# Optimization experiments

Measured on AMD Instinct MI355X. Metric: run time of the kernel, lower is better.

The kernel has to match this reference:

```python
import jax, jax.numpy as jnp
import numpy as np

GRID = 4096
WINDOW_SIZES = (128, 256, 512)  # self.window_schedule in the torch module
BLOCK_FRAC = 0.2                # fraction of blocked (fixed) cells


def setup_inputs() -> dict:
    key = jax.random.key(0)
    u = jax.random.uniform(key, (GRID, GRID), dtype=jnp.float32)
    # blocked cells > 0.0, free cells == 0.0 (binary fixed-cell occupancy mask)
    mask = (u > (1.0 - BLOCK_FRAC)).astype(jnp.float32)
    # the torch code requires the grid center (or an 8-neighbor) to be free;
    # force it free so the seed location is static.
    mask = mask.at[GRID // 2, GRID // 2].set(0.0)
    return {"fixed_cell_mask": mask}


def _dilate4(r):
    # 4-connected dilation of a boolean map (matches BFS neighbor set)
    up = jnp.pad(r[1:, :], ((0, 1), (0, 0)))
    dn = jnp.pad(r[:-1, :], ((1, 0), (0, 0)))
    lf = jnp.pad(r[:, 1:], ((0, 0), (0, 1)))
    rt = jnp.pad(r[:, :-1], ((0, 0), (1, 0)))
    return r | up | dn | lf | rt


def _flood_fill(free, cx, cy):
    """Parallel label-propagation equivalent of the serial BFS flood fill:
    reachable set of `free` cells 4-connected to seed (cx, cy). The seed is
    always tagged, exactly as in get_contiguous_free_region_in_window."""
    seed = jnp.zeros(free.shape, dtype=bool).at[cx, cy].set(True)

    def cond(state):
        reach, prev_count = state
        return jnp.sum(reach) != prev_count

    def body(state):
        reach, _ = state
        new = (_dilate4(reach) & free) | seed
        return new, jnp.sum(reach)

    reach, _ = jax.lax.while_loop(cond, body, (seed, jnp.int32(-1)))
    return reach


def reference(fixed_cell_mask):
    """Faithful JAX version of assemble_free_region_masks: for each window
    size, extract the centered window, flood-fill the contiguous free region
    from the center, and scatter it back into a full-grid boolean mask.
    Returns (masks [len(WINDOW_SIZES), H, W] float32, counts [len] int32)."""
    H, W = fixed_cell_mask.shape
    cx, cy = H // 2, W // 2  # seed is free by construction (see setup_inputs)
    masks, counts = [], []
    for size in WINDOW_SIZES:
        half = size // 2
        sx, ex = max(0, cx - half), min(H, cx + half)
        sy, ey = max(0, cy - half), min(W, cy + half)
        window = fixed_cell_mask[sx:ex, sy:ey]
        free = window == 0.0
        reach = _flood_fill(free, cx - sx, cy - sy)
        full = jnp.zeros((H, W), dtype=bool).at[sx:ex, sy:ey].set(reach)
        masks.append(full)
        counts.append(jnp.sum(reach))
    return jnp.stack(masks).astype(jnp.float32), jnp.stack(counts).astype(jnp.int32)
```

## Files before the change

kernel.cpp:

```cpp
#include <hip/hip_runtime.h>
#include <stdint.h>

#define GRID_N 4096
#define CELL_BLOCKS 1344
#define TILE_BLOCKS 336
#define NUM_EDGES 19712
#define EDGE_BLOCKS 77
#define ZERO_BLOCKS 8192

typedef float vfloat4 __attribute__((ext_vector_type(4)));

__device__ inline void decode_block(int b, int& w, int& S, int& lg, int& off,
                                    int& woff, int& baseblk) {
    if (b < 64)       { w = 0; S = 128; lg = 7; off = 1984; woff = 0;     baseblk = 0;   }
    else if (b < 320) { w = 1; S = 256; lg = 8; off = 1920; woff = 16384; baseblk = 64;  }
    else              { w = 2; S = 512; lg = 9; off = 1792; woff = 81920; baseblk = 320; }
}

__device__ inline void decode_tile(int b, int& S, int& lg, int& off, int& woff,
                                   int& tileR, int& tileC) {
    int t, tsh;
    if (b < 16)      { S = 128; lg = 7; off = 1984; woff = 0;     t = b;      tsh = 2; }
    else if (b < 80) { S = 256; lg = 8; off = 1920; woff = 16384; t = b - 16; tsh = 3; }
    else             { S = 512; lg = 9; off = 1792; woff = 81920; t = b - 80; tsh = 4; }
    tileR = t >> tsh;
    tileC = t & ((1 << tsh) - 1);
}

__device__ inline int uf_find(int* L, int a) {
    while (true) {
        int p = __hip_atomic_load(&L[a], __ATOMIC_RELAXED, __HIP_MEMORY_SCOPE_AGENT);
        if (p == a) return a;
        int gp = __hip_atomic_load(&L[p], __ATOMIC_RELAXED, __HIP_MEMORY_SCOPE_AGENT);
        if (gp == p) return p;
        __hip_atomic_compare_exchange_strong(&L[a], &p, gp,
            __ATOMIC_RELAXED, __ATOMIC_RELAXED, __HIP_MEMORY_SCOPE_AGENT);
        a = gp;
    }
}
__device__ inline void uf_union(int* L, int a, int b) {
    while (true) {
        a = uf_find(L, a);
        b = uf_find(L, b);
        if (a == b) return;
        if (a < b) { int t = a; a = b; b = t; }
        int old = atomicMin(&L[a], b);
        if (old == a) return;
        a = old;
    }
}

__device__ inline int lfind(int* lab, int a) {
    int p = __hip_atomic_load(&lab[a], __ATOMIC_RELAXED, __HIP_MEMORY_SCOPE_WORKGROUP);
    while (p != a) {
        a = p;
        p = __hip_atomic_load(&lab[a], __ATOMIC_RELAXED, __HIP_MEMORY_SCOPE_WORKGROUP);
    }
    return a;
}
__device__ inline void lunion(int* lab, int a, int b) {
    while (true) {
        a = lfind(lab, a);
        b = lfind(lab, b);
        if (a == b) return;
        if (a < b) { int t = a; a = b; b = t; }
        int old = atomicMin(&lab[a], b);
        if (old == a) return;
        a = old;
    }
}

__global__ void k_local(const float* __restrict__ mask, int* __restrict__ L) {
    int S, lg, off, woff, tileR, tileC;
    decode_tile(blockIdx.x, S, lg, off, woff, tileR, tileC);
    __shared__ int lab[1024];

    #pragma unroll
    for (int k = 0; k < 4; k++) {
        int l = threadIdx.x + k * 256;
        int lr = l >> 5, lc = l & 31;
        size_t g = (size_t)(off + tileR * 32 + lr) * GRID_N
                 + (size_t)(off + tileC * 32 + lc);
        lab[l] = (mask[g] == 0.0f) ? l : -1;
    }
    __syncthreads();

    #pragma unroll
    for (int k = 0; k < 4; k++) {
        int l = threadIdx.x + k * 256;
        if (lab[l] == -1) continue;
        int lr = l >> 5, lc = l & 31;
        if (lc + 1 < 32 && lab[l + 1] != -1)  lunion(lab, l, l + 1);
        if (lr + 1 < 32 && lab[l + 32] != -1) lunion(lab, l, l + 32);
    }
    __syncthreads();

    #pragma unroll
    for (int k = 0; k < 4; k++) {
        int l = threadIdx.x + k * 256;
        int lr = l >> 5, lc = l & 31;
        int gidx = (tileR * 32 + lr) * S + tileC * 32 + lc;
        if (lab[l] == -1) {
            L[woff + gidx] = -1;
        } else {
            int r = lfind(lab, l);
            int rr = r >> 5, rc = r & 31;
            L[woff + gidx] = (tileR * 32 + rr) * S + tileC * 32 + rc;
        }
    }
}

__global__ void k_zero_merge(int* __restrict__ L, float* __restrict__ out,
                             int out_size) {
    int b = blockIdx.x;
    if (b < EDGE_BLOCKS) {
        int e = b * 256 + threadIdx.x;
        int S, lg, woff, i; bool vert;
        if (e < 768)        { S = 128; lg = 7; woff = 0;     vert = e < 384;   i = vert ? e : e - 384; }
        else if (e < 4352)  { S = 256; lg = 8; woff = 16384; vert = e < 2560;  i = vert ? e - 768 : e - 2560; }
        else                { S = 512; lg = 9; woff = 81920; vert = e < 12032; i = vert ? e - 4352 : e - 12032; }
        int line = i >> lg;
        int pos = i & (S - 1);
        int* Lw = L + woff;
        int a, n;
        if (vert) { int c = line * 32 + 31; a = pos * S + c; n = a + 1; }
        else      { int r = line * 32 + 31; a = r * S + pos; n = a + S; }
        int la = Lw[a];
        int ln = Lw[n];
        int pla = __shfl_up(la, 1);
        int pln = __shfl_up(ln, 1);
        bool first = ((pos & 31) == 0);
        if (la != -1 && ln != -1 && (first || la != pla || ln != pln))
            uf_union(Lw, la, ln);
    } else {
        long long n4 = (long long)(out_size >> 2);
        long long i = (long long)(b - EDGE_BLOCKS) * 256 + threadIdx.x;
        long long stride = (long long)ZERO_BLOCKS * 256;
        vfloat4* o4 = (vfloat4*)out;
        vfloat4 z = (vfloat4)(0.0f);
        for (; i < n4; i += stride) __builtin_nontemporal_store(z, &o4[i]);
        long long t = (long long)(b - EDGE_BLOCKS) * 256 + threadIdx.x;
        long long tail = (long long)out_size - n4 * 4;
        if (t < tail) out[n4 * 4 + t] = 0.0f;
    }
}

__global__ void k_write(int* __restrict__ L, float* __restrict__ out) {
    int b = blockIdx.x;
    int w, S, lg, off, woff, baseblk;
    decode_block(b, w, S, lg, off, woff, baseblk);
    int idx = (b - baseblk) * 256 + threadIdx.x;
    int* Lw = L + woff;

    __shared__ int rootC;
    __shared__ float wsum[4];
    if (threadIdx.x == 0) {
        int centerIdx = (S >> 1) * S + (S >> 1);
        rootC = uf_find(Lw, centerIdx);
    }
    __syncthreads();

    int lab = Lw[idx];
    bool reach = false;
    if (lab != -1) {
        int root = uf_find(Lw, idx);
        reach = (root == rootC);
    }
    int r = idx >> lg;
    int c = idx & (S - 1);
    size_t go = (size_t)w * GRID_N * GRID_N + (size_t)(off + r) * GRID_N + (size_t)(off + c);
    out[go] = reach ? 1.0f : 0.0f;

    unsigned long long m = __ballot(reach);
    int lane = threadIdx.x & 63;
    int wv = threadIdx.x >> 6;
    if (lane == 0) wsum[wv] = (float)__popcll(m);
    __syncthreads();
    if (threadIdx.x == 0) {
        float s = wsum[0] + wsum[1] + wsum[2] + wsum[3];
        atomicAdd(&out[(size_t)3 * GRID_N * GRID_N + w], s);
    }
}

extern "C" void kernel_launch(void* const* d_in, const int* in_sizes, int n_in,
                              void* d_out, int out_size, void* d_ws, size_t ws_size,
                              hipStream_t stream) {
    const float* mask = (const float*)d_in[0];
    float* out = (float*)d_out;
    int* L = (int*)d_ws;

    k_local<<<TILE_BLOCKS, 256, 0, stream>>>(mask, L);
    k_zero_merge<<<EDGE_BLOCKS + ZERO_BLOCKS, 256, 0, stream>>>(L, out, out_size);
    k_write<<<CELL_BLOCKS, 256, 0, stream>>>(L, out);
}
```

Baseline: 274.3 us.

## Fuse CCL, merge, zero-fill and write into one cooperative kernel

Replaces the three separate launches with one cooperative kernel of 1024 blocks, using grid-wide syncs between the local labeling plus zero-fill phase, the edge merge phase and the write phase. It also adds path compression to the shared-memory find. The aim is to remove launch gaps and inter-kernel idle time. The trade-offs are fewer blocks doing the large zero-fill, the overhead of the grid barriers, and the cooperative launch's limit on residency.

```diff
diff --git a/kernel.cpp b/kernel.cpp
--- a/kernel.cpp
+++ b/kernel.cpp
@@ -1,14 +1,19 @@
 #include <hip/hip_runtime.h>
+#include <hip/hip_cooperative_groups.h>
 #include <stdint.h>
 
 #define GRID_N 4096
+#define NBLK 1024
+#define CCL_BLOCKS 336
 #define CELL_BLOCKS 1344
+#define NUM_EDGES 19712
 #define TILE_BLOCKS 336
-#define NUM_EDGES 19712
 #define EDGE_BLOCKS 77
 #define ZERO_BLOCKS 8192
 
 typedef float vfloat4 __attribute__((ext_vector_type(4)));
+
+namespace cg = cooperative_groups;
 
 __device__ inline void decode_block(int b, int& w, int& S, int& lg, int& off,
                                     int& woff, int& baseblk) {
@@ -51,12 +56,15 @@
 }
 
 __device__ inline int lfind(int* lab, int a) {
-    int p = __hip_atomic_load(&lab[a], __ATOMIC_RELAXED, __HIP_MEMORY_SCOPE_WORKGROUP);
-    while (p != a) {
-        a = p;
-        p = __hip_atomic_load(&lab[a], __ATOMIC_RELAXED, __HIP_MEMORY_SCOPE_WORKGROUP);
-    }
-    return a;
+    while (true) {
+        int p = __hip_atomic_load(&lab[a], __ATOMIC_RELAXED, __HIP_MEMORY_SCOPE_WORKGROUP);
+        if (p == a) return a;
+        int gp = __hip_atomic_load(&lab[p], __ATOMIC_RELAXED, __HIP_MEMORY_SCOPE_WORKGROUP);
+        if (gp == p) return p;
+        __hip_atomic_compare_exchange_strong(&lab[a], &p, gp,
+            __ATOMIC_RELAXED, __ATOMIC_RELAXED, __HIP_MEMORY_SCOPE_WORKGROUP);
+        a = gp;
+    }
 }
 __device__ inline void lunion(int* lab, int a, int b) {
     while (true) {
@@ -70,11 +78,124 @@
     }
 }
 
+__global__ __launch_bounds__(256, 4)
+void k_fused(const float* __restrict__ mask, int* __restrict__ L,
+             float* __restrict__ out, int out_size) {
+    __shared__ int lab[1024];
+    __shared__ int rootC;
+    __shared__ float wsum[4];
+    const int b = blockIdx.x;
+    const int tid = threadIdx.x;
+
+    if (b < CCL_BLOCKS) {
+        int S, lg, off, woff, tileR, tileC;
+        decode_tile(b, S, lg, off, woff, tileR, tileC);
+        (void)lg;
+        #pragma unroll
+        for (int k = 0; k < 4; k++) {
+            int l = tid + k * 256;
+            int lr = l >> 5, lc = l & 31;
+            size_t g = (size_t)(off + tileR * 32 + lr) * GRID_N
+                     + (size_t)(off + tileC * 32 + lc);
+            lab[l] = (mask[g] == 0.0f) ? l : -1;
+        }
+        __syncthreads();
+        #pragma unroll
+        for (int k = 0; k < 4; k++) {
+            int l = tid + k * 256;
+            if (lab[l] == -1) continue;
+            int lr = l >> 5, lc = l & 31;
+            if (lc + 1 < 32 && lab[l + 1] != -1)  lunion(lab, l, l + 1);
+            if (lr + 1 < 32 && lab[l + 32] != -1) lunion(lab, l, l + 32);
+        }
+        __syncthreads();
+        #pragma unroll
+        for (int k = 0; k < 4; k++) {
+            int l = tid + k * 256;
+            int lr = l >> 5, lc = l & 31;
+            int gidx = (tileR * 32 + lr) * S + tileC * 32 + lc;
+            if (lab[l] == -1) {
+                L[woff + gidx] = -1;
+            } else {
+                int r = lfind(lab, l);
+                int rr = r >> 5, rc = r & 31;
+                L[woff + gidx] = (tileR * 32 + rr) * S + tileC * 32 + rc;
+            }
+        }
+    } else {
+        long long n4 = (long long)(out_size >> 2);
+        long long i = (long long)(b - CCL_BLOCKS) * 256 + tid;
+        const long long stride = (long long)(NBLK - CCL_BLOCKS) * 256;
+        vfloat4* o4 = (vfloat4*)out;
+        vfloat4 z = (vfloat4)(0.0f);
+        for (; i < n4; i += stride) __builtin_nontemporal_store(z, &o4[i]);
+        long long t = (long long)(b - CCL_BLOCKS) * 256 + tid;
+        long long tail = (long long)out_size - n4 * 4;
+        if (t < tail) out[n4 * 4 + t] = 0.0f;
+    }
+    __threadfence();
+    cg::this_grid().sync();
+
+    {
+        int e = b * 256 + tid;
+        if (e < NUM_EDGES) {
+            int S, lg, woff, i; bool vert;
+            if (e < 768)        { S = 128; lg = 7; woff = 0;     vert = e < 384;   i = vert ? e : e - 384; }
+            else if (e < 4352)  { S = 256; lg = 8; woff = 16384; vert = e < 2560;  i = vert ? e - 768 : e - 2560; }
+            else                { S = 512; lg = 9; woff = 81920; vert = e < 12032; i = vert ? e - 4352 : e - 12032; }
+            int line = i >> lg;
+            int pos = i & (S - 1);
+            int* Lw = L + woff;
+            int a, n;
+            if (vert) { int c = line * 32 + 31; a = pos * S + c; n = a + 1; }
+            else      { int r = line * 32 + 31; a = r * S + pos; n = a + S; }
+            int la = Lw[a];
+            int ln = Lw[n];
+            int pla = __shfl_up(la, 1);
+            int pln = __shfl_up(ln, 1);
+            bool first = ((pos & 31) == 0);
+            if (la != -1 && ln != -1 && (first || la != pla || ln != pln))
+                uf_union(Lw, la, ln);
+        }
+    }
+    __threadfence();
+    cg::this_grid().sync();
+
+    for (int vb = b; vb < CELL_BLOCKS; vb += NBLK) {
+        int w, S, lg, off, woff, baseblk;
+        decode_block(vb, w, S, lg, off, woff, baseblk);
+        int idx = (vb - baseblk) * 256 + tid;
+        int* Lw = L + woff;
+        if (tid == 0) {
+            int centerIdx = (S >> 1) * S + (S >> 1);
+            rootC = uf_find(Lw, centerIdx);
+        }
+        __syncthreads();
+        int lb = Lw[idx];
+        bool reach = false;
+        if (lb != -1) reach = (uf_find(Lw, lb) == rootC);
+        int r = idx >> lg;
+        int c = idx & (S - 1);
+        size_t go = (size_t)w * GRID_N * GRID_N + (size_t)(off + r) * GRID_N + (size_t)(off + c);
+        out[go] = reach ? 1.0f : 0.0f;
+        unsigned long long m = __ballot(reach);
+        int lane = tid & 63;
+        int wv = tid >> 6;
+        if (lane == 0) wsum[wv] = (float)__popcll(m);
+        __syncthreads();
+        if (tid == 0) {
+            float s = wsum[0] + wsum[1] + wsum[2] + wsum[3];
+            atomicAdd(&out[(size_t)3 * GRID_N * GRID_N + w], s);
+        }
+        __syncthreads();
+    }
+}
+
 __global__ void k_local(const float* __restrict__ mask, int* __restrict__ L) {
     int S, lg, off, woff, tileR, tileC;
     decode_tile(blockIdx.x, S, lg, off, woff, tileR, tileC);
+    (void)lg;
     __shared__ int lab[1024];
-
     #pragma unroll
     for (int k = 0; k < 4; k++) {
         int l = threadIdx.x + k * 256;
@@ -84,7 +205,6 @@
         lab[l] = (mask[g] == 0.0f) ? l : -1;
     }
     __syncthreads();
-
     #pragma unroll
     for (int k = 0; k < 4; k++) {
         int l = threadIdx.x + k * 256;
@@ -94,7 +214,6 @@
         if (lr + 1 < 32 && lab[l + 32] != -1) lunion(lab, l, l + 32);
     }
     __syncthreads();
-
     #pragma unroll
     for (int k = 0; k < 4; k++) {
         int l = threadIdx.x + k * 256;
@@ -151,7 +270,6 @@
     decode_block(b, w, S, lg, off, woff, baseblk);
     int idx = (b - baseblk) * 256 + threadIdx.x;
     int* Lw = L + woff;
-
     __shared__ int rootC;
     __shared__ float wsum[4];
     if (threadIdx.x == 0) {
@@ -159,18 +277,13 @@
         rootC = uf_find(Lw, centerIdx);
     }
     __syncthreads();
-
-    int lab = Lw[idx];
+    int lb = Lw[idx];
     bool reach = false;
-    if (lab != -1) {
-        int root = uf_find(Lw, idx);
-        reach = (root == rootC);
-    }
+    if (lb != -1) reach = (uf_find(Lw, lb) == rootC);
     int r = idx >> lg;
     int c = idx & (S - 1);
     size_t go = (size_t)w * GRID_N * GRID_N + (size_t)(off + r) * GRID_N + (size_t)(off + c);
     out[go] = reach ? 1.0f : 0.0f;
-
     unsigned long long m = __ballot(reach);
     int lane = threadIdx.x & 63;
     int wv = threadIdx.x >> 6;
@@ -188,8 +301,15 @@
     const float* mask = (const float*)d_in[0];
     float* out = (float*)d_out;
     int* L = (int*)d_ws;
-
-    k_local<<<TILE_BLOCKS, 256, 0, stream>>>(mask, L);
-    k_zero_merge<<<EDGE_BLOCKS + ZERO_BLOCKS, 256, 0, stream>>>(L, out, out_size);
-    k_write<<<CELL_BLOCKS, 256, 0, stream>>>(L, out);
-}
+    int osz = out_size;
+
+    void* args[] = { (void*)&mask, (void*)&L, (void*)&out, (void*)&osz };
+    hipError_t err = hipLaunchCooperativeKernel((const void*)k_fused,
+                                                dim3(NBLK), dim3(256),
+                                                args, 0u, stream);
+    if (err != hipSuccess) {
+        k_local<<<TILE_BLOCKS, 256, 0, stream>>>(mask, L);
+        k_zero_merge<<<EDGE_BLOCKS + ZERO_BLOCKS, 256, 0, stream>>>(L, out, osz);
+        k_write<<<CELL_BLOCKS, 256, 0, stream>>>(L, out);
+    }
+}
```

Result: slower. 686.6 us (+150.3%).

## Fuse output zeroing with local CCL kernel and dedupe root finds per wavefront

Applied to the files above, without the earlier changes.

Moves the large output-zeroing pass into the same launch as the per-tile connected-component labelling, so the memory-bound zero fill overlaps with the compute-bound tile CCL. Edge merging now gets its own small kernel. In the write kernel, each wavefront now runs one union-find per distinct label and broadcasts the root with shuffles, instead of every lane calling uf_find. This cuts redundant atomic loads at the cost of a serial loop over distinct labels per wave.

```diff
diff --git a/kernel.cpp b/kernel.cpp
--- a/kernel.cpp
+++ b/kernel.cpp
@@ -2,11 +2,12 @@
 #include <stdint.h>
 
 #define GRID_N 4096
+#define CCL_BLOCKS 336
+#define ZERO_BLOCKS 8192
+#define K1_BLOCKS (CCL_BLOCKS + ZERO_BLOCKS)
 #define CELL_BLOCKS 1344
-#define TILE_BLOCKS 336
 #define NUM_EDGES 19712
 #define EDGE_BLOCKS 77
-#define ZERO_BLOCKS 8192
 
 typedef float vfloat4 __attribute__((ext_vector_type(4)));
 
@@ -70,79 +71,80 @@
     }
 }
 
-__global__ void k_local(const float* __restrict__ mask, int* __restrict__ L) {
-    int S, lg, off, woff, tileR, tileC;
-    decode_tile(blockIdx.x, S, lg, off, woff, tileR, tileC);
-    __shared__ int lab[1024];
-
-    #pragma unroll
-    for (int k = 0; k < 4; k++) {
-        int l = threadIdx.x + k * 256;
-        int lr = l >> 5, lc = l & 31;
-        size_t g = (size_t)(off + tileR * 32 + lr) * GRID_N
-                 + (size_t)(off + tileC * 32 + lc);
-        lab[l] = (mask[g] == 0.0f) ? l : -1;
-    }
-    __syncthreads();
-
-    #pragma unroll
-    for (int k = 0; k < 4; k++) {
-        int l = threadIdx.x + k * 256;
-        if (lab[l] == -1) continue;
-        int lr = l >> 5, lc = l & 31;
-        if (lc + 1 < 32 && lab[l + 1] != -1)  lunion(lab, l, l + 1);
-        if (lr + 1 < 32 && lab[l + 32] != -1) lunion(lab, l, l + 32);
-    }
-    __syncthreads();
-
-    #pragma unroll
-    for (int k = 0; k < 4; k++) {
-        int l = threadIdx.x + k * 256;
-        int lr = l >> 5, lc = l & 31;
-        int gidx = (tileR * 32 + lr) * S + tileC * 32 + lc;
-        if (lab[l] == -1) {
-            L[woff + gidx] = -1;
-        } else {
-            int r = lfind(lab, l);
-            int rr = r >> 5, rc = r & 31;
-            L[woff + gidx] = (tileR * 32 + rr) * S + tileC * 32 + rc;
+__global__ void k_ccl_zero(const float* __restrict__ mask, int* __restrict__ L,
+                           float* __restrict__ out, int out_size) {
+    const int b = blockIdx.x;
+    if (b < CCL_BLOCKS) {
+        int S, lg, off, woff, tileR, tileC;
+        decode_tile(b, S, lg, off, woff, tileR, tileC);
+        (void)lg;
+        __shared__ int lab[1024];
+
+        #pragma unroll
+        for (int k = 0; k < 4; k++) {
+            int l = threadIdx.x + k * 256;
+            int lr = l >> 5, lc = l & 31;
+            size_t g = (size_t)(off + tileR * 32 + lr) * GRID_N
+                     + (size_t)(off + tileC * 32 + lc);
+            lab[l] = (mask[g] == 0.0f) ? l : -1;
         }
-    }
-}
-
-__global__ void k_zero_merge(int* __restrict__ L, float* __restrict__ out,
-                             int out_size) {
-    int b = blockIdx.x;
-    if (b < EDGE_BLOCKS) {
-        int e = b * 256 + threadIdx.x;
-        int S, lg, woff, i; bool vert;
-        if (e < 768)        { S = 128; lg = 7; woff = 0;     vert = e < 384;   i = vert ? e : e - 384; }
-        else if (e < 4352)  { S = 256; lg = 8; woff = 16384; vert = e < 2560;  i = vert ? e - 768 : e - 2560; }
-        else                { S = 512; lg = 9; woff = 81920; vert = e < 12032; i = vert ? e - 4352 : e - 12032; }
-        int line = i >> lg;
-        int pos = i & (S - 1);
-        int* Lw = L + woff;
-        int a, n;
-        if (vert) { int c = line * 32 + 31; a = pos * S + c; n = a + 1; }
-        else      { int r = line * 32 + 31; a = r * S + pos; n = a + S; }
-        int la = Lw[a];
-        int ln = Lw[n];
-        int pla = __shfl_up(la, 1);
-        int pln = __shfl_up(ln, 1);
-        bool first = ((pos & 31) == 0);
-        if (la != -1 && ln != -1 && (first || la != pla || ln != pln))
-            uf_union(Lw, la, ln);
+        __syncthreads();
+
+        #pragma unroll
+        for (int k = 0; k < 4; k++) {
+            int l = threadIdx.x + k * 256;
+            if (lab[l] == -1) continue;
+            int lr = l >> 5, lc = l & 31;
+            if (lc + 1 < 32 && lab[l + 1] != -1)  lunion(lab, l, l + 1);
+            if (lr + 1 < 32 && lab[l + 32] != -1) lunion(lab, l, l + 32);
+        }
+        __syncthreads();
+
+        #pragma unroll
+        for (int k = 0; k < 4; k++) {
+            int l = threadIdx.x + k * 256;
+            int lr = l >> 5, lc = l & 31;
+            int gidx = (tileR * 32 + lr) * S + tileC * 32 + lc;
+            if (lab[l] == -1) {
+                L[woff + gidx] = -1;
+            } else {
+                int r = lfind(lab, l);
+                int rr = r >> 5, rc = r & 31;
+                L[woff + gidx] = (tileR * 32 + rr) * S + tileC * 32 + rc;
+            }
+        }
     } else {
         long long n4 = (long long)(out_size >> 2);
-        long long i = (long long)(b - EDGE_BLOCKS) * 256 + threadIdx.x;
-        long long stride = (long long)ZERO_BLOCKS * 256;
+        long long i = (long long)(b - CCL_BLOCKS) * 256 + threadIdx.x;
+        const long long stride = (long long)ZERO_BLOCKS * 256;
         vfloat4* o4 = (vfloat4*)out;
         vfloat4 z = (vfloat4)(0.0f);
         for (; i < n4; i += stride) __builtin_nontemporal_store(z, &o4[i]);
-        long long t = (long long)(b - EDGE_BLOCKS) * 256 + threadIdx.x;
+        long long t = (long long)(b - CCL_BLOCKS) * 256 + threadIdx.x;
         long long tail = (long long)out_size - n4 * 4;
         if (t < tail) out[n4 * 4 + t] = 0.0f;
     }
+}
+
+__global__ void k_edges(int* __restrict__ L) {
+    int e = blockIdx.x * 256 + threadIdx.x;
+    int S, lg, woff, i; bool vert;
+    if (e < 768)        { S = 128; lg = 7; woff = 0;     vert = e < 384;   i = vert ? e : e - 384; }
+    else if (e < 4352)  { S = 256; lg = 8; woff = 16384; vert = e < 2560;  i = vert ? e - 768 : e - 2560; }
+    else                { S = 512; lg = 9; woff = 81920; vert = e < 12032; i = vert ? e - 4352 : e - 12032; }
+    int line = i >> lg;
+    int pos = i & (S - 1);
+    int* Lw = L + woff;
+    int a, n;
+    if (vert) { int c = line * 32 + 31; a = pos * S + c; n = a + 1; }
+    else      { int r = line * 32 + 31; a = r * S + pos; n = a + S; }
+    int la = Lw[a];
+    int ln = Lw[n];
+    int pla = __shfl_up(la, 1);
+    int pln = __shfl_up(ln, 1);
+    bool first = ((pos & 31) == 0);
+    if (la != -1 && ln != -1 && (first || la != pla || ln != pln))
+        uf_union(Lw, la, ln);
 }
 
 __global__ void k_write(int* __restrict__ L, float* __restrict__ out) {
@@ -160,12 +162,21 @@
     }
     __syncthreads();
 
-    int lab = Lw[idx];
-    bool reach = false;
-    if (lab != -1) {
-        int root = uf_find(Lw, idx);
-        reach = (root == rootC);
-    }
+    int lb = Lw[idx];
+    int root = -1;
+    unsigned long long need = __ballot(lb != -1);
+    while (need) {
+        int leader = __builtin_ctzll(need);
+        int llab = __shfl(lb, leader);
+        int lroot = 0;
+        if ((threadIdx.x & 63) == leader) lroot = uf_find(Lw, llab);
+        lroot = __shfl(lroot, leader);
+        bool match = (lb == llab);
+        if (match) root = lroot;
+        need &= ~__ballot(match);
+    }
+    bool reach = (lb != -1) && (root == rootC);
+
     int r = idx >> lg;
     int c = idx & (S - 1);
     size_t go = (size_t)w * GRID_N * GRID_N + (size_t)(off + r) * GRID_N + (size_t)(off + c);
@@ -189,7 +200,7 @@
     float* out = (float*)d_out;
     int* L = (int*)d_ws;
 
-    k_local<<<TILE_BLOCKS, 256, 0, stream>>>(mask, L);
-    k_zero_merge<<<EDGE_BLOCKS + ZERO_BLOCKS, 256, 0, stream>>>(L, out, out_size);
+    k_ccl_zero<<<K1_BLOCKS, 256, 0, stream>>>(mask, L, out, out_size);
+    k_edges<<<EDGE_BLOCKS, 256, 0, stream>>>(L);
     k_write<<<CELL_BLOCKS, 256, 0, stream>>>(L, out);
 }
```

Result: no change. 269.0 us (-1.9%).
